# Kernel optimization log

Measured on AMD Instinct MI355X. Metric: run time of the kernel, lower is better.

The kernel has to match this reference:

```python
import jax, jax.numpy as jnp
import numpy as np

N_NODES = 50000
N_EDGES = 800000
NODE_IN = 5
EDGE_IN = 1
HID = 64


def setup_inputs() -> dict:
    key = jax.random.key(0)
    ks = jax.random.split(key, 16)
    x = jax.random.normal(ks[0], (N_NODES, NODE_IN), dtype=jnp.float32)
    edge_index = jax.random.randint(ks[1], (2, N_EDGES), 0, N_NODES, dtype=jnp.int32)
    edge_attr = jax.random.normal(ks[2], (N_EDGES, EDGE_IN), dtype=jnp.float32)
    def lin(k, fan_in, fan_out):
        b = 1.0 / np.sqrt(fan_in)
        k1, k2 = jax.random.split(k)
        W = jax.random.uniform(k1, (fan_in, fan_out), minval=-b, maxval=b, dtype=jnp.float32)
        bi = jax.random.uniform(k2, (fan_out,), minval=-b, maxval=b, dtype=jnp.float32)
        return W, bi
    W_ne, b_ne = lin(ks[3], NODE_IN, HID)
    W_ee, b_ee = lin(ks[4], EDGE_IN, HID)
    W_gcn, b_gcn = lin(ks[5], HID, HID)   # PyG GCNConv: lin (no bias) + separate bias
    W1, b1 = lin(ks[6], 3 * HID, HID)
    W2, b2 = lin(ks[7], HID, 1)
    return {"x": x, "edge_index": edge_index, "edge_attr": edge_attr,
            "W_ne": W_ne, "b_ne": b_ne, "W_ee": W_ee, "b_ee": b_ee,
            "W_gcn": W_gcn, "b_gcn": b_gcn, "W1": W1, "b1": b1, "W2": W2, "b2": b2}


def gcn_conv(h, edge_index, W, b):
    # PyG GCNConv: add self-loops, symmetric norm D^-1/2 (A+I) D^-1/2, linear, scatter-add.
    N = h.shape[0]
    src, dst = edge_index[0], edge_index[1]
    loops = jnp.arange(N, dtype=src.dtype)
    row = jnp.concatenate([src, loops])  # message sources
    col = jnp.concatenate([dst, loops])  # message targets
    deg = jax.ops.segment_sum(jnp.ones(col.shape[0], h.dtype), col, num_segments=N)
    dinv = jnp.where(deg > 0, jax.lax.rsqrt(deg), 0.0)
    norm = dinv[row] * dinv[col]          # [E+N]
    ht = h @ W                            # [N, HID]
    msg = ht[row] * norm[:, None]         # gather + scale
    return jax.ops.segment_sum(msg, col, num_segments=N) + b


def reference(x, edge_index, edge_attr, W_ne, b_ne, W_ee, b_ee, W_gcn, b_gcn, W1, b1, W2, b2):
    h = jax.nn.relu(x @ W_ne + b_ne)                    # node encoder
    ef = jax.nn.relu(edge_attr @ W_ee + b_ee)           # edge encoder
    h = gcn_conv(h, edge_index, W_gcn, b_gcn)           # GCN layer
    src, dst = edge_index[0], edge_index[1]
    edge_input = jnp.concatenate([h[src], h[dst], ef], axis=1)  # [E, 3*HID]
    out = jax.nn.relu(edge_input @ W1 + b1) @ W2 + b2   # edge MLP -> [E, 1]
    return out.reshape(-1)
```

## Files before the change

### kernel.cpp

```cpp
#include <hip/hip_runtime.h>

#define NN 50000
#define NE 800000
#define H  64
#define NBKT 196
#define BCAP 8192
#define BIN_CHUNK 2048

typedef __attribute__((ext_vector_type(8))) short bf16x8;
typedef __attribute__((ext_vector_type(4))) float f32x4;

__device__ __forceinline__ unsigned short f2bf(float f) {
  unsigned int u = __builtin_bit_cast(unsigned int, f);
  u += 0x7FFFu + ((u >> 16) & 1u);
  return (unsigned short)(u >> 16);
}
__device__ __forceinline__ float bf2f(unsigned short u) {
  unsigned int v = ((unsigned int)u) << 16;
  return __builtin_bit_cast(float, v);
}

__global__ __launch_bounds__(256) void k_prep(
    const float* __restrict__ W1, const float* __restrict__ b1,
    const float* __restrict__ W_ee, const float* __restrict__ b_ee,
    float* __restrict__ thrS, float* __restrict__ cT,
    unsigned short* __restrict__ w1f, int* __restrict__ gcur) {
  const int t = threadIdx.x;
  if (blockIdx.x == 2) {
    if (t < NBKT) gcur[t] = 0;
    return;
  }
  if (blockIdx.x == 1) {
    const int ln = t & 63, q = t >> 6;
    const int l15_ = ln & 15, l4_ = ln >> 4;
#pragma unroll
    for (int f = 0; f < 4; ++f) {
      const int idx = q * 4 + f;
      const int g = idx >> 3;
      const int ct = (idx >> 1) & 3;
      const int c = idx & 1;
#pragma unroll
      for (int j = 0; j < 8; ++j) {
        const int k = g * 64 + c * 32 + l4_ * 8 + j;
        const int hcol = ct * 16 + l15_;
        w1f[(idx * 64 + ln) * 8 + j] = f2bf(W1[k * H + hcol]);
      }
    }
    return;
  }
  __shared__ float swee[64], sbee[64], sth[64];
  __shared__ int skx[64];
  if (t < 64) {
    const float w = W_ee[t], b = b_ee[t];
    swee[t] = w; sbee[t] = b;
    sth[t] = (w != 0.f) ? (-b / w) : __builtin_inff();
    skx[t] = t;
  }
  __syncthreads();
  for (int sz = 2; sz <= 64; sz <<= 1)
    for (int st = sz >> 1; st > 0; st >>= 1) {
      if (t < 64) {
        const int p = t ^ st;
        if (p > t) {
          const bool up = ((t & sz) == 0);
          const float a = sth[t], bb = sth[p];
          if (up ? (a > bb) : (a < bb)) {
            const int ka = skx[t];
            sth[t] = bb; sth[p] = a;
            skx[t] = skx[p]; skx[p] = ka;
          }
        }
      }
      __syncthreads();
    }
  if (t < 64) {
    const int h = t;
    float c1 = 0.f, c0 = b1[h];
    for (int k = 0; k < 64; ++k) {
      const float w = swee[k], b = sbee[k];
      if (w < 0.f || (w == 0.f && b > 0.f)) {
        const float wv1 = W1[(128 + k) * H + h];
        c1 = fmaf(w, wv1, c1);
        c0 = fmaf(b, wv1, c0);
      }
    }
    float2* cT2 = (float2*)cT;
    cT2[h] = make_float2(c1, c0);
    for (int iv = 1; iv <= 64; ++iv) {
      const int ks = skx[iv - 1];
      const float w = swee[ks];
      const float s = (w > 0.f) ? 1.f : -1.f;
      const float wv1 = W1[(128 + ks) * H + h];
      c1 = fmaf(s * w, wv1, c1);
      c0 = fmaf(s * sbee[ks], wv1, c0);
      cT2[iv * 66 + h] = make_float2(c1, c0);
    }
    thrS[h] = sth[h];
  }
}

__global__ __launch_bounds__(256) void k_bin(const int* __restrict__ ei,
                                             unsigned int* __restrict__ gbin,
                                             int* __restrict__ gcur) {
  __shared__ int hist[NBKT], base[NBKT];
  const int t = threadIdx.x;
  if (t < NBKT) hist[t] = 0;
  __syncthreads();

  const int e0 = blockIdx.x * BIN_CHUNK;
  int srcv[8], dstv[8], loff[8];
#pragma unroll
  for (int j = 0; j < 8; ++j) {
    const int e = e0 + j * 256 + t;
    if (e < NE) {
      srcv[j] = ei[e];
      dstv[j] = ei[NE + e];
      loff[j] = atomicAdd(&hist[dstv[j] >> 8], 1);
    } else dstv[j] = -1;
  }
  __syncthreads();
  if (t < NBKT) base[t] = atomicAdd(&gcur[t], hist[t]);
  __syncthreads();
#pragma unroll
  for (int j = 0; j < 8; ++j) {
    if (dstv[j] >= 0) {
      const int b = dstv[j] >> 8;
      const int pos = base[b] + loff[j];
      if (pos < BCAP)
        gbin[(size_t)b * BCAP + pos] =
            ((unsigned int)srcv[j] << 8) | (unsigned int)(dstv[j] & 255);
    }
  }
}

__global__ __launch_bounds__(256) void k_pass2(const unsigned int* __restrict__ gbin,
                                               const int* __restrict__ gcur,
                                               unsigned short* __restrict__ gcsr,
                                               int2* __restrict__ rowrange,
                                               float* __restrict__ dinv) {
  __shared__ int hist[256], cur[256], sc[256];
  __shared__ unsigned short lcsr[BCAP];
  const int b = blockIdx.x, t = threadIdx.x;
  const int sz = min(gcur[b], BCAP);
  hist[t] = 0;
  __syncthreads();

  const unsigned int* bb = gbin + (size_t)b * BCAP;
  unsigned int ent[32];
#pragma unroll
  for (int k = 0; k < 32; ++k) {
    const int i = t + k * 256;
    if (i < sz) {
      ent[k] = bb[i];
      atomicAdd(&hist[ent[k] & 255], 1);
    }
  }
  __syncthreads();

  int v = hist[t];
  const int cnt = v;
  sc[t] = v;
  __syncthreads();
#pragma unroll
  for (int off = 1; off < 256; off <<= 1) {
    const int o = (t >= off) ? sc[t - off] : 0;
    __syncthreads();
    v += o;
    sc[t] = v;
    __syncthreads();
  }
  const int ex = v - cnt;
  cur[t] = ex;
  const int d = b * 256 + t;
  if (d < NN) {
    const int beg = b * BCAP + ex;
    rowrange[d] = make_int2(beg, beg + cnt);
    dinv[d] = rsqrtf((float)(cnt + 1));
  }
  __syncthreads();

#pragma unroll
  for (int k = 0; k < 32; ++k) {
    const int i = t + k * 256;
    if (i < sz) {
      const unsigned int en = ent[k];
      const int off = atomicAdd(&cur[en & 255], 1);
      lcsr[off] = (unsigned short)(en >> 8);
    }
  }
  __syncthreads();
  for (int i = t; i < sz; i += 256) gcsr[(size_t)b * BCAP + i] = lcsr[i];
}

__global__ __launch_bounds__(256) void k_node(
    const float* __restrict__ x, const float* __restrict__ W_ne,
    const float* __restrict__ b_ne, const float* __restrict__ W_gcn,
    const float* __restrict__ dinv, unsigned short* __restrict__ htb) {
  __shared__ float sh[4][H];
  const int lane = threadIdx.x & 63;
  const int wv   = threadIdx.x >> 6;
  const int n    = blockIdx.x * 4 + wv;

  float acc = b_ne[lane];
#pragma unroll
  for (int k = 0; k < 5; ++k) acc = fmaf(x[n * 5 + k], W_ne[k * H + lane], acc);
  acc = fmaxf(acc, 0.0f);
  sh[wv][lane] = acc;
  __syncthreads();

  float hv = 0.0f;
#pragma unroll 8
  for (int k = 0; k < H; ++k) hv = fmaf(sh[wv][k], W_gcn[k * H + lane], hv);

  htb[(size_t)n * H + lane] = f2bf(hv * dinv[n]);
}

__global__ __launch_bounds__(256) void k_gather_uv(
    const int2* __restrict__ rowrange, const unsigned short* __restrict__ gcsr,
    const unsigned short* __restrict__ htb, const float* __restrict__ dinv,
    const float* __restrict__ b_gcn, const unsigned short* __restrict__ w1f,
    unsigned short* __restrict__ u, unsigned short* __restrict__ v) {
  __shared__ unsigned short shg[16 * 64];
  const int lane = threadIdx.x & 63;
  const int wv   = threadIdx.x >> 6;
  const int n0   = blockIdx.x * 16;
  const float bg = b_gcn[lane];

#pragma unroll 1
  for (int q = 0; q < 4; ++q) {
    const int nl = wv * 4 + q;
    const int n  = n0 + nl;
    const int2 rr = rowrange[n];
    float sum = bf2f(htb[(size_t)n * H + lane]);
    int i = rr.x;
#pragma unroll 1
    for (; i + 4 <= rr.y; i += 4) {
      const int s0 = gcsr[i], s1 = gcsr[i + 1];
      const int s2 = gcsr[i + 2], s3 = gcsr[i + 3];
      const float v0 = bf2f(htb[(size_t)s0 * H + lane]);
      const float v1 = bf2f(htb[(size_t)s1 * H + lane]);
      const float v2 = bf2f(htb[(size_t)s2 * H + lane]);
      const float v3 = bf2f(htb[(size_t)s3 * H + lane]);
      sum += (v0 + v1) + (v2 + v3);
    }
#pragma unroll 1
    for (; i < rr.y; ++i) sum += bf2f(htb[(size_t)gcsr[i] * H + lane]);

    const float hgv = fmaf(dinv[n], sum, bg);
    shg[((nl * 128 + lane * 2) ^ ((nl & 7) << 4)) >> 1] = f2bf(hgv);
  }
  __syncthreads();

  const int l15 = lane & 15, l4 = lane >> 4;
  const bf16x8 a0 = *(const bf16x8*)(shg + (((l15 * 128 + l4 * 16) ^ ((l15 & 7) << 4)) >> 1));
  const bf16x8 a1 = *(const bf16x8*)(shg + (((l15 * 128 + 64 + l4 * 16) ^ ((l15 & 7) << 4)) >> 1));

  const int ct = wv;
  const bf16x8 bu0 = *(const bf16x8*)(w1f + ((ct * 2 + 0) * 64 + lane) * 8);
  const bf16x8 bu1 = *(const bf16x8*)(w1f + ((ct * 2 + 1) * 64 + lane) * 8);
  const bf16x8 bv0 = *(const bf16x8*)(w1f + ((8 + ct * 2 + 0) * 64 + lane) * 8);
  const bf16x8 bv1 = *(const bf16x8*)(w1f + ((8 + ct * 2 + 1) * 64 + lane) * 8);

  f32x4 au = (f32x4)(0.f), av = (f32x4)(0.f);
  au = __builtin_amdgcn_mfma_f32_16x16x32_bf16(a0, bu0, au, 0, 0, 0);
  au = __builtin_amdgcn_mfma_f32_16x16x32_bf16(a1, bu1, au, 0, 0, 0);
  av = __builtin_amdgcn_mfma_f32_16x16x32_bf16(a0, bv0, av, 0, 0, 0);
  av = __builtin_amdgcn_mfma_f32_16x16x32_bf16(a1, bv1, av, 0, 0, 0);

#pragma unroll
  for (int r = 0; r < 4; ++r) {
    const size_t idx = (size_t)(n0 + l4 * 4 + r) * H + ct * 16 + l15;
    u[idx] = f2bf(au[r]);
    v[idx] = f2bf(av[r]);
  }
}

__device__ __forceinline__ int find_iv(const float* __restrict__ sThr, float ea) {
  int iv = 0;
#pragma unroll
  for (int st = 64; st >= 1; st >>= 1) {
    const int nc = iv + st;
    if (nc <= 64 && sThr[nc - 1] <= ea) iv = nc;
  }
  return iv;
}

__device__ __forceinline__ void edge_compute(
    float ea, uint4 U0, uint4 U1, uint4 V0, uint4 V1,
    const float* __restrict__ sThr, const float* __restrict__ sCT,
    const float* __restrict__ w2v, int l4, int lane, float b2v,
    float* __restrict__ out, int obase) {
  const int iv = find_iv(sThr, ea);
  const float* cp = sCT + iv * 132 + l4 * 32;
  const unsigned int ud[8] = {U0.x, U0.y, U0.z, U0.w, U1.x, U1.y, U1.z, U1.w};
  const unsigned int vd[8] = {V0.x, V0.y, V0.z, V0.w, V1.x, V1.y, V1.z, V1.w};
  float p = 0.f;
#pragma unroll
  for (int r = 0; r < 8; ++r) {
    const float4 cc = *(const float4*)(cp + r * 4);
    const float ulo = __builtin_bit_cast(float, ud[r] << 16);
    const float uhi = __builtin_bit_cast(float, ud[r] & 0xFFFF0000u);
    const float vlo = __builtin_bit_cast(float, vd[r] << 16);
    const float vhi = __builtin_bit_cast(float, vd[r] & 0xFFFF0000u);
    const float z0 = ulo + vlo + fmaf(ea, cc.x, cc.y);
    const float z1 = uhi + vhi + fmaf(ea, cc.z, cc.w);
    p = fmaf(fmaxf(z0, 0.f), w2v[2 * r], p);
    p = fmaf(fmaxf(z1, 0.f), w2v[2 * r + 1], p);
  }
  p += __shfl_xor(p, 16);
  p += __shfl_xor(p, 32);
  if (lane < 16) out[obase + lane] = p + b2v;
}

#define ET 5
__global__ __launch_bounds__(512) void k_edge(
    const int* __restrict__ ei, const float* __restrict__ eattr,
    const unsigned short* __restrict__ u, const unsigned short* __restrict__ v,
    const float* __restrict__ thrS, const float* __restrict__ cT,
    const float* __restrict__ W2, const float* __restrict__ b2,
    float* __restrict__ out) {
  __shared__ float sThr[64];
  __shared__ float sCT[65 * 132];

  const int t = threadIdx.x;
  if (t < 64) sThr[t] = thrS[t];
  for (int i = t; i < 65 * 66; i += 512)
    ((float2*)sCT)[i] = ((const float2*)cT)[i];
  __syncthreads();

  const int lane = t & 63;
  const int wv   = t >> 6;
  const int l15  = lane & 15, l4 = lane >> 4;
  const float b2v = b2[0];

  float w2v[16];
#pragma unroll
  for (int j = 0; j < 16; ++j) w2v[j] = W2[l4 * 16 + j];

  const int tile0 = (blockIdx.x * 8 + wv) * ET;
  int srcA[ET], dstA[ET];
  float eaA[ET];
#pragma unroll
  for (int tt = 0; tt < ET; ++tt) {
    srcA[tt] = ei[(tile0 + tt) * 16 + l15];
    dstA[tt] = ei[NE + (tile0 + tt) * 16 + l15];
    eaA[tt]  = eattr[(tile0 + tt) * 16 + l15];
  }

  uint4 Au0, Au1, Av0, Av1, Bu0, Bu1, Bv0, Bv1;

#define LOADUV(U0, U1, V0, V1, tt) {                              \
    const unsigned short* up = u + (size_t)srcA[tt] * H + l4 * 16; \
    const unsigned short* vp = v + (size_t)dstA[tt] * H + l4 * 16; \
    U0 = *(const uint4*)(up); U1 = *(const uint4*)(up + 8);        \
    V0 = *(const uint4*)(vp); V1 = *(const uint4*)(vp + 8); }

  LOADUV(Au0, Au1, Av0, Av1, 0);
  LOADUV(Bu0, Bu1, Bv0, Bv1, 1);
  edge_compute(eaA[0], Au0, Au1, Av0, Av1, sThr, sCT, w2v, l4, lane, b2v, out, (tile0 + 0) * 16);
  LOADUV(Au0, Au1, Av0, Av1, 2);
  edge_compute(eaA[1], Bu0, Bu1, Bv0, Bv1, sThr, sCT, w2v, l4, lane, b2v, out, (tile0 + 1) * 16);
  LOADUV(Bu0, Bu1, Bv0, Bv1, 3);
  edge_compute(eaA[2], Au0, Au1, Av0, Av1, sThr, sCT, w2v, l4, lane, b2v, out, (tile0 + 2) * 16);
  LOADUV(Au0, Au1, Av0, Av1, 4);
  edge_compute(eaA[3], Bu0, Bu1, Bv0, Bv1, sThr, sCT, w2v, l4, lane, b2v, out, (tile0 + 3) * 16);
  edge_compute(eaA[4], Au0, Au1, Av0, Av1, sThr, sCT, w2v, l4, lane, b2v, out, (tile0 + 4) * 16);
#undef LOADUV
}

extern "C" void kernel_launch(void* const* d_in, const int* in_sizes, int n_in,
                              void* d_out, int out_size, void* d_ws, size_t ws_size,
                              hipStream_t stream) {
  const float* x     = (const float*)d_in[0];
  const int*   ei    = (const int*)d_in[1];
  const float* eattr = (const float*)d_in[2];
  const float* W_ne  = (const float*)d_in[3];
  const float* b_ne  = (const float*)d_in[4];
  const float* W_ee  = (const float*)d_in[5];
  const float* b_ee  = (const float*)d_in[6];
  const float* W_gcn = (const float*)d_in[7];
  const float* b_gcn = (const float*)d_in[8];
  const float* W1    = (const float*)d_in[9];
  const float* b1    = (const float*)d_in[10];
  const float* W2    = (const float*)d_in[11];
  const float* b2    = (const float*)d_in[12];
  float* out = (float*)d_out;

  char* ws = (char*)d_ws;
  unsigned short* htb = (unsigned short*)(ws + 0);
  unsigned short* uT  = (unsigned short*)(ws + 6400000);
  unsigned int*   gbin = (unsigned int*)(ws + 12800000);
  unsigned short* vT  = (unsigned short*)(ws + 12800000);
  unsigned short* gcsr = (unsigned short*)(ws + 19222528);
  int2*  rowrange = (int2*)(ws + 22433792);
  float* dinv    = (float*)(ws + 22833792);
  int*   gcur    = (int*)(ws + 23033792);
  float* thrS    = (float*)(ws + 23034592);
  float* cT      = (float*)(ws + 23034848);
  unsigned short* w1f = (unsigned short*)(ws + 23069168);

  k_prep<<<3, 256, 0, stream>>>(W1, b1, W_ee, b_ee, thrS, cT, w1f, gcur);
  k_bin<<<(NE + BIN_CHUNK - 1) / BIN_CHUNK, 256, 0, stream>>>(ei, gbin, gcur);
  k_pass2<<<NBKT, 256, 0, stream>>>(gbin, gcur, gcsr, rowrange, dinv);
  k_node<<<NN / 4, 256, 0, stream>>>(x, W_ne, b_ne, W_gcn, dinv, htb);
  k_gather_uv<<<NN / 16, 256, 0, stream>>>(rowrange, gcsr, htb, dinv, b_gcn, w1f, uT, vT);
  k_edge<<<NE / (8 * ET * 16), 512, 0, stream>>>(ei, eattr, uT, vT, thrS, cT, W2, b2, out);
}
```

Measured before the change: 153.8 us.

## Fold prep kernel into binning kernel, pad edge LUT, unroll gather by eight

Merges the small prep kernel into the binning kernel as two extra blocks and replaces the counter reset with a memset, cutting one kernel launch from the chain. The per-interval coefficient table is re-laid out as float4 rows padded to 37 per interval (9 per lane group), which is meant to reduce LDS bank conflicts in the edge kernel. The CSR gather loop is unrolled from 4 to 8 neighbours to keep more loads in flight. The memset adds a small launch of its own, and the w1f offset moves to fit the larger table.

```diff
diff --git a/kernel.cpp b/kernel.cpp
--- a/kernel.cpp
+++ b/kernel.cpp
@@ -6,6 +6,8 @@
 #define NBKT 196
 #define BCAP 8192
 #define BIN_CHUNK 2048
+#define NBIN (NE + BIN_CHUNK - 1) / BIN_CHUNK
+#define CT4N (65 * 37)
 
 typedef __attribute__((ext_vector_type(8))) short bf16x8;
 typedef __attribute__((ext_vector_type(4))) float f32x4;
@@ -20,17 +22,16 @@
   return __builtin_bit_cast(float, v);
 }
 
-__global__ __launch_bounds__(256) void k_prep(
+__global__ __launch_bounds__(256) void k_bin(
+    const int* __restrict__ ei, unsigned int* __restrict__ gbin,
+    int* __restrict__ gcur,
     const float* __restrict__ W1, const float* __restrict__ b1,
     const float* __restrict__ W_ee, const float* __restrict__ b_ee,
     float* __restrict__ thrS, float* __restrict__ cT,
-    unsigned short* __restrict__ w1f, int* __restrict__ gcur) {
+    unsigned short* __restrict__ w1f) {
   const int t = threadIdx.x;
-  if (blockIdx.x == 2) {
-    if (t < NBKT) gcur[t] = 0;
-    return;
-  }
-  if (blockIdx.x == 1) {
+
+  if (blockIdx.x == NBIN + 1) {
     const int ln = t & 63, q = t >> 6;
     const int l15_ = ln & 15, l4_ = ln >> 4;
 #pragma unroll
@@ -48,62 +49,65 @@
     }
     return;
   }
-  __shared__ float swee[64], sbee[64], sth[64];
-  __shared__ int skx[64];
-  if (t < 64) {
-    const float w = W_ee[t], b = b_ee[t];
-    swee[t] = w; sbee[t] = b;
-    sth[t] = (w != 0.f) ? (-b / w) : __builtin_inff();
-    skx[t] = t;
-  }
-  __syncthreads();
-  for (int sz = 2; sz <= 64; sz <<= 1)
-    for (int st = sz >> 1; st > 0; st >>= 1) {
-      if (t < 64) {
-        const int p = t ^ st;
-        if (p > t) {
-          const bool up = ((t & sz) == 0);
-          const float a = sth[t], bb = sth[p];
-          if (up ? (a > bb) : (a < bb)) {
-            const int ka = skx[t];
-            sth[t] = bb; sth[p] = a;
-            skx[t] = skx[p]; skx[p] = ka;
+
+  if (blockIdx.x == NBIN) {
+    __shared__ float swee[64], sbee[64], sth[64];
+    __shared__ int skx[64];
+    if (t < 64) {
+      const float w = W_ee[t], b = b_ee[t];
+      swee[t] = w; sbee[t] = b;
+      sth[t] = (w != 0.f) ? (-b / w) : __builtin_inff();
+      skx[t] = t;
+    }
+    __syncthreads();
+    for (int sz = 2; sz <= 64; sz <<= 1)
+      for (int st = sz >> 1; st > 0; st >>= 1) {
+        if (t < 64) {
+          const int p = t ^ st;
+          if (p > t) {
+            const bool up = ((t & sz) == 0);
+            const float a = sth[t], bb = sth[p];
+            if (up ? (a > bb) : (a < bb)) {
+              const int ka = skx[t];
+              sth[t] = bb; sth[p] = a;
+              skx[t] = skx[p]; skx[p] = ka;
+            }
           }
         }
+        __syncthreads();
       }
-      __syncthreads();
-    }
-  if (t < 64) {
-    const int h = t;
-    float c1 = 0.f, c0 = b1[h];
-    for (int k = 0; k < 64; ++k) {
-      const float w = swee[k], b = sbee[k];
-      if (w < 0.f || (w == 0.f && b > 0.f)) {
-        const float wv1 = W1[(128 + k) * H + h];
-        c1 = fmaf(w, wv1, c1);
-        c0 = fmaf(b, wv1, c0);
+    if (t < 64) {
+      const int h = t;
+      const int l4h = h >> 4, rh = (h & 15) >> 1, sub = h & 1;
+      float c1 = 0.f, c0 = b1[h];
+      for (int k = 0; k < 64; ++k) {
+        const float w = swee[k], b = sbee[k];
+        if (w < 0.f || (w == 0.f && b > 0.f)) {
+          const float wv1 = W1[(128 + k) * H + h];
+          c1 = fmaf(w, wv1, c1);
+          c0 = fmaf(b, wv1, c0);
+        }
       }
-    }
-    float2* cT2 = (float2*)cT;
-    cT2[h] = make_float2(c1, c0);
-    for (int iv = 1; iv <= 64; ++iv) {
-      const int ks = skx[iv - 1];
-      const float w = swee[ks];
-      const float s = (w > 0.f) ? 1.f : -1.f;
-      const float wv1 = W1[(128 + ks) * H + h];
-      c1 = fmaf(s * w, wv1, c1);
-      c0 = fmaf(s * sbee[ks], wv1, c0);
-      cT2[iv * 66 + h] = make_float2(c1, c0);
-    }
-    thrS[h] = sth[h];
-  }
-}
-
-__global__ __launch_bounds__(256) void k_bin(const int* __restrict__ ei,
-                                             unsigned int* __restrict__ gbin,
-                                             int* __restrict__ gcur) {
+      {
+        float* base = cT + (size_t)(0 * 37 + l4h * 9 + rh) * 4;
+        base[2 * sub] = c1; base[2 * sub + 1] = c0;
+      }
+      for (int iv = 1; iv <= 64; ++iv) {
+        const int ks = skx[iv - 1];
+        const float w = swee[ks];
+        const float s = (w > 0.f) ? 1.f : -1.f;
+        const float wv1 = W1[(128 + ks) * H + h];
+        c1 = fmaf(s * w, wv1, c1);
+        c0 = fmaf(s * sbee[ks], wv1, c0);
+        float* base = cT + (size_t)(iv * 37 + l4h * 9 + rh) * 4;
+        base[2 * sub] = c1; base[2 * sub + 1] = c0;
+      }
+      thrS[h] = sth[h];
+    }
+    return;
+  }
+
   __shared__ int hist[NBKT], base[NBKT];
-  const int t = threadIdx.x;
   if (t < NBKT) hist[t] = 0;
   __syncthreads();
 
@@ -234,14 +238,20 @@
     float sum = bf2f(htb[(size_t)n * H + lane]);
     int i = rr.x;
 #pragma unroll 1
-    for (; i + 4 <= rr.y; i += 4) {
-      const int s0 = gcsr[i], s1 = gcsr[i + 1];
+    for (; i + 8 <= rr.y; i += 8) {
+      const int s0 = gcsr[i],     s1 = gcsr[i + 1];
       const int s2 = gcsr[i + 2], s3 = gcsr[i + 3];
+      const int s4 = gcsr[i + 4], s5 = gcsr[i + 5];
+      const int s6 = gcsr[i + 6], s7 = gcsr[i + 7];
       const float v0 = bf2f(htb[(size_t)s0 * H + lane]);
       const float v1 = bf2f(htb[(size_t)s1 * H + lane]);
       const float v2 = bf2f(htb[(size_t)s2 * H + lane]);
       const float v3 = bf2f(htb[(size_t)s3 * H + lane]);
-      sum += (v0 + v1) + (v2 + v3);
+      const float v4 = bf2f(htb[(size_t)s4 * H + lane]);
+      const float v5 = bf2f(htb[(size_t)s5 * H + lane]);
+      const float v6 = bf2f(htb[(size_t)s6 * H + lane]);
+      const float v7 = bf2f(htb[(size_t)s7 * H + lane]);
+      sum += ((v0 + v1) + (v2 + v3)) + ((v4 + v5) + (v6 + v7));
     }
 #pragma unroll 1
     for (; i < rr.y; ++i) sum += bf2f(htb[(size_t)gcsr[i] * H + lane]);
@@ -287,17 +297,17 @@
 
 __device__ __forceinline__ void edge_compute(
     float ea, uint4 U0, uint4 U1, uint4 V0, uint4 V1,
-    const float* __restrict__ sThr, const float* __restrict__ sCT,
+    const float* __restrict__ sThr, const float4* __restrict__ sCT4,
     const float* __restrict__ w2v, int l4, int lane, float b2v,
     float* __restrict__ out, int obase) {
   const int iv = find_iv(sThr, ea);
-  const float* cp = sCT + iv * 132 + l4 * 32;
+  const float4* cp = sCT4 + iv * 37 + l4 * 9;
   const unsigned int ud[8] = {U0.x, U0.y, U0.z, U0.w, U1.x, U1.y, U1.z, U1.w};
   const unsigned int vd[8] = {V0.x, V0.y, V0.z, V0.w, V1.x, V1.y, V1.z, V1.w};
   float p = 0.f;
 #pragma unroll
   for (int r = 0; r < 8; ++r) {
-    const float4 cc = *(const float4*)(cp + r * 4);
+    const float4 cc = cp[r];
     const float ulo = __builtin_bit_cast(float, ud[r] << 16);
     const float uhi = __builtin_bit_cast(float, ud[r] & 0xFFFF0000u);
     const float vlo = __builtin_bit_cast(float, vd[r] << 16);
@@ -320,12 +330,14 @@
     const float* __restrict__ W2, const float* __restrict__ b2,
     float* __restrict__ out) {
   __shared__ float sThr[64];
-  __shared__ float sCT[65 * 132];
+  __shared__ float4 sCT4[CT4N];
 
   const int t = threadIdx.x;
   if (t < 64) sThr[t] = thrS[t];
-  for (int i = t; i < 65 * 66; i += 512)
-    ((float2*)sCT)[i] = ((const float2*)cT)[i];
+  {
+    const float4* g = (const float4*)cT;
+    for (int i = t; i < CT4N; i += 512) sCT4[i] = g[i];
+  }
   __syncthreads();
 
   const int lane = t & 63;
@@ -349,7 +361,7 @@
 
   uint4 Au0, Au1, Av0, Av1, Bu0, Bu1, Bv0, Bv1;
 
-#define LOADUV(U0, U1, V0, V1, tt) {                              \
+#define LOADUV(U0, U1, V0, V1, tt) {                               \
     const unsigned short* up = u + (size_t)srcA[tt] * H + l4 * 16; \
     const unsigned short* vp = v + (size_t)dstA[tt] * H + l4 * 16; \
     U0 = *(const uint4*)(up); U1 = *(const uint4*)(up + 8);        \
@@ -357,14 +369,14 @@
 
   LOADUV(Au0, Au1, Av0, Av1, 0);
   LOADUV(Bu0, Bu1, Bv0, Bv1, 1);
-  edge_compute(eaA[0], Au0, Au1, Av0, Av1, sThr, sCT, w2v, l4, lane, b2v, out, (tile0 + 0) * 16);
+  edge_compute(eaA[0], Au0, Au1, Av0, Av1, sThr, sCT4, w2v, l4, lane, b2v, out, (tile0 + 0) * 16);
   LOADUV(Au0, Au1, Av0, Av1, 2);
-  edge_compute(eaA[1], Bu0, Bu1, Bv0, Bv1, sThr, sCT, w2v, l4, lane, b2v, out, (tile0 + 1) * 16);
+  edge_compute(eaA[1], Bu0, Bu1, Bv0, Bv1, sThr, sCT4, w2v, l4, lane, b2v, out, (tile0 + 1) * 16);
   LOADUV(Bu0, Bu1, Bv0, Bv1, 3);
-  edge_compute(eaA[2], Au0, Au1, Av0, Av1, sThr, sCT, w2v, l4, lane, b2v, out, (tile0 + 2) * 16);
+  edge_compute(eaA[2], Au0, Au1, Av0, Av1, sThr, sCT4, w2v, l4, lane, b2v, out, (tile0 + 2) * 16);
   LOADUV(Au0, Au1, Av0, Av1, 4);
-  edge_compute(eaA[3], Bu0, Bu1, Bv0, Bv1, sThr, sCT, w2v, l4, lane, b2v, out, (tile0 + 3) * 16);
-  edge_compute(eaA[4], Au0, Au1, Av0, Av1, sThr, sCT, w2v, l4, lane, b2v, out, (tile0 + 4) * 16);
+  edge_compute(eaA[3], Bu0, Bu1, Bv0, Bv1, sThr, sCT4, w2v, l4, lane, b2v, out, (tile0 + 3) * 16);
+  edge_compute(eaA[4], Au0, Au1, Av0, Av1, sThr, sCT4, w2v, l4, lane, b2v, out, (tile0 + 4) * 16);
 #undef LOADUV
 }
 
@@ -397,10 +409,10 @@
   int*   gcur    = (int*)(ws + 23033792);
   float* thrS    = (float*)(ws + 23034592);
   float* cT      = (float*)(ws + 23034848);
-  unsigned short* w1f = (unsigned short*)(ws + 23069168);
-
-  k_prep<<<3, 256, 0, stream>>>(W1, b1, W_ee, b_ee, thrS, cT, w1f, gcur);
-  k_bin<<<(NE + BIN_CHUNK - 1) / BIN_CHUNK, 256, 0, stream>>>(ei, gbin, gcur);
+  unsigned short* w1f = (unsigned short*)(ws + 23073328);
+
+  hipMemsetAsync(gcur, 0, NBKT * sizeof(int), stream);
+  k_bin<<<NBIN + 2, 256, 0, stream>>>(ei, gbin, gcur, W1, b1, W_ee, b_ee, thrS, cT, w1f);
   k_pass2<<<NBKT, 256, 0, stream>>>(gbin, gcur, gcsr, rowrange, dinv);
   k_node<<<NN / 4, 256, 0, stream>>>(x, W_ne, b_ne, W_gcn, dinv, htb);
   k_gather_uv<<<NN / 16, 256, 0, stream>>>(rowrange, gcsr, htb, dinv, b_gcn, w1f, uT, vT);
```

Result: faster. 148.7 us (-3.3%).
